# Performance work log

Measured on AMD Instinct MI355X. Metric: run time of the kernel, lower is better.

The kernel has to match this reference:

```python
import jax, jax.numpy as jnp
import numpy as np

NUM_EMBEDDINGS = 8192
EMBEDDING_DIM = 256
COMMITMENT_COST = 0.25


def setup_inputs() -> dict:
    key = jax.random.key(0)
    k1, k2 = jax.random.split(key)
    inputs = jax.random.normal(k1, (32, 32, 32, EMBEDDING_DIM), dtype=jnp.float32)
    # flax nn.initializers.uniform(scale=1/num_embeddings) -> U[0, scale)
    embeddings = jax.random.uniform(
        k2, (NUM_EMBEDDINGS, EMBEDDING_DIM), dtype=jnp.float32,
        minval=0.0, maxval=1.0 / NUM_EMBEDDINGS)
    return {"inputs": inputs, "embeddings": embeddings}


def reference(inputs, embeddings):
    flat_input = inputs.reshape(-1, EMBEDDING_DIM)  # [N, D]
    distances = (jnp.sum(flat_input ** 2, axis=1, keepdims=True)
                 - 2.0 * jnp.dot(flat_input, embeddings.T)
                 + jnp.sum(embeddings ** 2, axis=1)[None, :])
    encoding_indices = jnp.argmin(distances, axis=1)  # [N]
    quantized = embeddings[encoding_indices]  # [N, D]

    e_latent_loss = jnp.mean((jax.lax.stop_gradient(quantized) - flat_input) ** 2)
    q_latent_loss = jnp.mean((quantized - jax.lax.stop_gradient(flat_input)) ** 2)
    vq_loss = q_latent_loss + COMMITMENT_COST * e_latent_loss

    # straight-through estimator
    quantized_st = flat_input + jax.lax.stop_gradient(quantized - flat_input)
    quantized_st = quantized_st.reshape(inputs.shape)

    # perplexity via codebook usage histogram (avoids materializing one-hot)
    counts = jnp.zeros((NUM_EMBEDDINGS,), dtype=flat_input.dtype).at[encoding_indices].add(1.0)
    avg_probs = counts / flat_input.shape[0]
    perplexity = jnp.exp(-jnp.sum(avg_probs * jnp.log(avg_probs + 1e-10)))

    return quantized_st, vq_loss, perplexity, encoding_indices
```

## Files before the change

kernel.cpp:

```cpp
#include <hip/hip_runtime.h>
#include <math.h>

#pragma clang fp contract(off)

#define N_ROWS 32768
#define DIM    256
#define K_EMB  8192
#define BCAP   2048
#define NSUB   256

typedef float  f32x4  __attribute__((ext_vector_type(4)));
typedef short  bf16x8 __attribute__((ext_vector_type(8)));

__device__ __forceinline__ void gl_lds16(const uint4* g, uint4* l) {
  __builtin_amdgcn_global_load_lds(
      (const __attribute__((address_space(1))) unsigned int*)g,
      (__attribute__((address_space(3))) unsigned int*)l,
      16, 0, 0);
}

__device__ __forceinline__ unsigned bf_rne(float f) {
  unsigned u = __float_as_uint(f);
  return (u + 0x7fffu + ((u >> 16) & 1u)) >> 16;
}
__device__ __forceinline__ unsigned pack2(float lo, float hi) {
  return bf_rne(lo) | (bf_rne(hi) << 16);
}

__device__ __forceinline__ float np_pw128_sumsq(const float* __restrict__ a) {
  float4 v0 = *(const float4*)(a);
  float4 v1 = *(const float4*)(a + 4);
  float r0 = v0.x*v0.x, r1 = v0.y*v0.y, r2 = v0.z*v0.z, r3 = v0.w*v0.w;
  float r4 = v1.x*v1.x, r5 = v1.y*v1.y, r6 = v1.z*v1.z, r7 = v1.w*v1.w;
  for (int i = 8; i < 128; i += 8) {
    float4 w0 = *(const float4*)(a + i);
    float4 w1 = *(const float4*)(a + i + 4);
    r0 += w0.x*w0.x; r1 += w0.y*w0.y; r2 += w0.z*w0.z; r3 += w0.w*w0.w;
    r4 += w1.x*w1.x; r5 += w1.y*w1.y; r6 += w1.z*w1.z; r7 += w1.w*w1.w;
  }
  return ((r0+r1)+(r2+r3))+((r4+r5)+(r6+r7));
}

__global__ __launch_bounds__(256) void vq_sumsq(const float* __restrict__ src,
                                                float* __restrict__ dst, int nrows) {
  int gid  = blockIdx.x * 256 + threadIdx.x;
  int row  = gid >> 1, half = gid & 1;
  if (row >= nrows) return;
  float s = np_pw128_sumsq(src + (size_t)row * DIM + half * 128);
  float o = __shfl_xor(s, 1);
  if (half == 0) dst[row] = s + o;
}

__global__ __launch_bounds__(256) void vq_init(unsigned* __restrict__ hist,
                                               unsigned* __restrict__ bcnt,
                                               unsigned* __restrict__ ovf,
                                               unsigned long long* __restrict__ best) {
  int i = blockIdx.x * 256 + threadIdx.x;
  ovf[i]  = 0u;
  best[i] = ~0ull;
  if (i < K_EMB) hist[i] = 0u;
  if (i < NSUB)  bcnt[i] = 0u;
}

__global__ __launch_bounds__(256) void vq_cvt_frag(const float* __restrict__ E,
                                                   uint4* __restrict__ Eb) {
  int t = blockIdx.x * 256 + threadIdx.x;
  int tile = t >> 6, l = t & 63;
  int cfg = tile >> 3, ks = tile & 7;
  int code = cfg * 16 + (l & 15);
  int k0 = (ks * 4 + (l >> 4)) * 8;
  const float4* src = (const float4*)(E + (size_t)code * DIM + k0);
  float4 a = src[0], b = src[1];
  uint4 o;
  o.x = pack2(a.x, a.y); o.y = pack2(a.z, a.w);
  o.z = pack2(b.x, b.y); o.w = pack2(b.z, b.w);
  Eb[t] = o;
}

__global__ __launch_bounds__(512)
__attribute__((amdgpu_waves_per_eu(4, 4)))
void vq_mfma_slice(
    const float* __restrict__ X, const uint4* __restrict__ Eb,
    unsigned short* __restrict__ submax_g) {
  __shared__ __align__(16) unsigned short es[64 * 256];
  __shared__ unsigned short sh[2][64][128];

  const int tid   = threadIdx.x;
  const int lane  = tid & 63, w = tid >> 6;
  const int lr    = lane & 15, lg = lane >> 4;
  const int wcg   = w & 1;
  const int wxg   = w >> 1;
  const int rb    = blockIdx.x >> 1;
  const int slice = blockIdx.x & 1;
  const int row0  = rb * 128;

  bf16x8 bx[2][8];
#pragma unroll
  for (int cf = 0; cf < 2; ++cf) {
    const float* xr = X + (size_t)(row0 + wxg * 32 + cf * 16 + lr) * DIM;
#pragma unroll
    for (int ks = 0; ks < 8; ++ks) {
      int k0 = (ks * 4 + lg) * 8;
      float4 a = *(const float4*)(xr + k0);
      float4 b = *(const float4*)(xr + k0 + 4);
      uint4 o;
      o.x = pack2(a.x, a.y); o.y = pack2(a.z, a.w);
      o.z = pack2(b.x, b.y); o.w = pack2(b.z, b.w);
      bx[cf][ks] = *(bf16x8*)&o;
    }
  }

  const uint4* ebase = Eb + (size_t)slice * 131072;

  for (int c = 0; c < 64; ++c) {
    __syncthreads();
#pragma unroll
    for (int i = 0; i < 4; ++i) {
      int u = tid + i * 512;
      gl_lds16(ebase + (size_t)c * 2048 + u, ((uint4*)es) + u);
    }
    __syncthreads();

    f32x4 acc[2][2];
#pragma unroll
    for (int rf = 0; rf < 2; ++rf)
#pragma unroll
      for (int cf = 0; cf < 2; ++cf)
        acc[rf][cf] = (f32x4){0.f, 0.f, 0.f, 0.f};

#pragma unroll
    for (int ks = 0; ks < 8; ++ks) {
      bf16x8 ev0 = *(const bf16x8*)(es + (((wcg * 2 + 0) * 8 + ks) * 64 + lane) * 8);
      bf16x8 ev1 = *(const bf16x8*)(es + (((wcg * 2 + 1) * 8 + ks) * 64 + lane) * 8);
      acc[0][0] = __builtin_amdgcn_mfma_f32_16x16x32_bf16(ev0, bx[0][ks], acc[0][0], 0, 0, 0);
      acc[0][1] = __builtin_amdgcn_mfma_f32_16x16x32_bf16(ev0, bx[1][ks], acc[0][1], 0, 0, 0);
      acc[1][0] = __builtin_amdgcn_mfma_f32_16x16x32_bf16(ev1, bx[0][ks], acc[1][0], 0, 0, 0);
      acc[1][1] = __builtin_amdgcn_mfma_f32_16x16x32_bf16(ev1, bx[1][ks], acc[1][1], 0, 0, 0);
    }

#pragma unroll
    for (int cf = 0; cf < 2; ++cf) {
      float m = acc[0][cf][0];
#pragma unroll
      for (int rf = 0; rf < 2; ++rf)
#pragma unroll
        for (int rg = 0; rg < 4; ++rg)
          if (rf | rg) m = fmaxf(m, acc[rf][cf][rg]);
      m = fmaxf(m, __shfl_xor(m, 16));
      m = fmaxf(m, __shfl_xor(m, 32));
      if (lg == 0) {
        int qi = (int)((m + 0.0625f) * 524288.0f);
        qi = qi < 0 ? 0 : (qi > 65535 ? 65535 : qi);
        sh[wcg][c][wxg * 32 + cf * 16 + lr] = (unsigned short)qi;
      }
    }
  }
  __syncthreads();

  {
    int r = tid & 127, g = tid >> 7;
    unsigned short* dst = submax_g + (size_t)(row0 + r) * NSUB + slice * 128 + g * 32;
#pragma unroll
    for (int i = 0; i < 32; ++i) {
      int sl = g * 32 + i;
      dst[i] = sh[sl & 1][sl >> 1][r];
    }
  }
}

__global__ __launch_bounds__(256) void vq_flag(
    const unsigned short* __restrict__ submax_g, const float* __restrict__ A,
    unsigned* __restrict__ bcnt, unsigned short* __restrict__ buckets,
    unsigned* __restrict__ ovf) {
  __shared__ unsigned cntA[NSUB], baseS[NSUB], cntC[NSUB];
  const int t   = threadIdx.x;
  const int row = blockIdx.x * 256 + t;
  cntA[t] = 0u; cntC[t] = 0u;
  __syncthreads();

  const unsigned short* sr = submax_g + (size_t)row * NSUB;
  int mq = 0;
  for (int s = 0; s < NSUB; ++s) {
    int q = sr[s];
    mq = q > mq ? q : mq;
  }
  const int wq   = (int)((sqrtf(A[row]) * 4e-6f + 9.6e-5f) * 524288.0f) + 2;
  const int thrq = mq - wq;

  for (int s = 0; s < NSUB; ++s)
    if ((int)sr[s] >= thrq) atomicAdd(&cntA[s], 1u);
  __syncthreads();

  baseS[t] = atomicAdd(&bcnt[t], cntA[t]);
  __syncthreads();

  for (int s = 0; s < NSUB; ++s) {
    if ((int)sr[s] >= thrq) {
      unsigned p = baseS[s] + atomicAdd(&cntC[s], 1u);
      if (p < BCAP) buckets[s * BCAP + p] = (unsigned short)row;
      else          ovf[row] = 1u;
    }
  }
}

__global__ __launch_bounds__(256) void vq_exact(
    const float* __restrict__ X, const float* __restrict__ E,
    const float* __restrict__ A, const float* __restrict__ C,
    const unsigned* __restrict__ bcnt, const unsigned short* __restrict__ buckets,
    unsigned long long* __restrict__ best) {
  __shared__ float e_lds[32][260];
  __shared__ float xr[4][4][256];
  const int tid  = threadIdx.x;
  const int lane = tid & 63, w = tid >> 6;
  const int bk   = blockIdx.x >> 2, q4 = blockIdx.x & 3;

#pragma unroll
  for (int i = 0; i < 8; ++i) {
    int u = tid + i * 256;
    int code = u >> 6, koff = (u & 63) * 4;
    float4 v = *(const float4*)(E + (size_t)(bk * 32 + code) * DIM + koff);
    *(float4*)(&e_lds[code][koff]) = v;
  }
  __syncthreads();

  int n = (int)bcnt[bk]; if (n > BCAP) n = BCAP;
  const int   half = lane >> 5, c32 = lane & 31;
  const int   j  = bk * 32 + c32;
  const float cj = C[j];

  for (int p0 = q4 * 16 + w * 4; p0 < n; p0 += 64) {
    int valid[4], rows[4];
#pragma unroll
    for (int k = 0; k < 4; ++k) {
      int pk = p0 + k;
      valid[k] = (pk < n);
      rows[k]  = buckets[(size_t)bk * BCAP + (pk < n ? pk : p0)];
    }
#pragma unroll
    for (int k = 0; k < 4; ++k)
      *(float4*)(&xr[w][k][lane * 4]) =
          *(const float4*)(X + (size_t)rows[k] * DIM + lane * 4);
    asm volatile("s_waitcnt lgkmcnt(0)" ::: "memory");

    float acc0 = 0.f, acc1 = 0.f;
    const float* xa = &xr[w][half][0];
    const float* xb = &xr[w][half + 2][0];
#pragma unroll 4
    for (int kq = 0; kq < 64; ++kq) {
      float4 ev = *(const float4*)(&e_lds[c32][kq * 4]);
      float4 x0 = *(const float4*)(xa + kq * 4);
      float4 x1 = *(const float4*)(xb + kq * 4);
      acc0 = fmaf(x0.x, ev.x, acc0); acc0 = fmaf(x0.y, ev.y, acc0);
      acc0 = fmaf(x0.z, ev.z, acc0); acc0 = fmaf(x0.w, ev.w, acc0);
      acc1 = fmaf(x1.x, ev.x, acc1); acc1 = fmaf(x1.y, ev.y, acc1);
      acc1 = fmaf(x1.z, ev.z, acc1); acc1 = fmaf(x1.w, ev.w, acc1);
    }
    float d0 = (A[rows[half]]     - 2.0f * acc0) + cj;
    float d1 = (A[rows[half + 2]] - 2.0f * acc1) + cj;
    int   j0 = j, j1 = j;
#pragma unroll
    for (int mm = 1; mm < 32; mm <<= 1) {
      float od = __shfl_xor(d0, mm); int oj = __shfl_xor(j0, mm);
      if (od < d0 || (od == d0 && oj < j0)) { d0 = od; j0 = oj; }
      od = __shfl_xor(d1, mm); oj = __shfl_xor(j1, mm);
      if (od < d1 || (od == d1 && oj < j1)) { d1 = od; j1 = oj; }
    }
    if (c32 == 0) {
      if (valid[half])
        atomicMin(&best[rows[half]],
                  ((unsigned long long)__float_as_uint(d0) << 32) | (unsigned)j0);
      if (valid[half + 2])
        atomicMin(&best[rows[half + 2]],
                  ((unsigned long long)__float_as_uint(d1) << 32) | (unsigned)j1);
    }
  }
}

__global__ __launch_bounds__(256) void vq_finish(
    const float* __restrict__ X, const float* __restrict__ E,
    const float* __restrict__ A, const float* __restrict__ C,
    const unsigned* __restrict__ ovf, const unsigned long long* __restrict__ best,
    int* __restrict__ idx_out, float* __restrict__ idxf_out) {
  int row  = blockIdx.x * 4 + (threadIdx.x >> 6);
  int lane = threadIdx.x & 63;
  if (!ovf[row]) {
    if (lane == 0) {
      int j = (int)(best[row] & 0xffffffffu);
      idx_out[row]  = j;
      idxf_out[row] = (float)j;
    }
    return;
  }
  const float a_r = A[row];
  const float4* X4 = (const float4*)(X + (size_t)row * DIM);
  float bd = INFINITY; int bj = 0x7fffffff;
  for (int j = lane; j < K_EMB; j += 64) {
    const float4* E4 = (const float4*)(E + (size_t)j * DIM);
    float acc = 0.f;
    for (int kb = 0; kb < 64; ++kb) {
      float4 xv = X4[kb], ev = E4[kb];
      acc = fmaf(xv.x, ev.x, acc); acc = fmaf(xv.y, ev.y, acc);
      acc = fmaf(xv.z, ev.z, acc); acc = fmaf(xv.w, ev.w, acc);
    }
    float d = (a_r - 2.0f * acc) + C[j];
    if (d < bd || (d == bd && j < bj)) { bd = d; bj = j; }
  }
  for (int m = 1; m < 64; m <<= 1) {
    float od = __shfl_xor(bd, m);
    int   oj = __shfl_xor(bj, m);
    if (od < bd || (od == bd && oj < bj)) { bd = od; bj = oj; }
  }
  if (lane == 0) { idx_out[row] = bj; idxf_out[row] = (float)bj; }
}

__global__ __launch_bounds__(256) void vq_argmin(const float* __restrict__ X,
                                                 const float* __restrict__ E,
                                                 const float* __restrict__ A,
                                                 const float* __restrict__ C,
                                                 int* __restrict__ idx_out,
                                                 float* __restrict__ idxf_out) {
  __shared__ float4 xs4[64 * 64];
  const int tid  = threadIdx.x;
  const int rl   = tid >> 2;
  const int cg   = tid & 3;
  const int row0 = blockIdx.x * 64;

  const float4* Xg = (const float4*)(X + (size_t)row0 * DIM);
  for (int it = 0; it < 16; ++it) {
    int f4 = tid + it * 256;
    float4 v = Xg[f4];
    int r = f4 >> 6, kb = f4 & 63;
    xs4[r * 64 + (kb ^ (r & 7))] = v;
  }
  __syncthreads();

  const float a_r = A[row0 + rl];
  const int   swq = rl & 7;
  const float4* xrow = xs4 + rl * 64;

  float bd = INFINITY;
  int   bj = 0x7fffffff;

  for (int tile = 0; tile < K_EMB; tile += 16) {
    const int j0 = tile + cg * 4;
    const float4* e0 = (const float4*)(E + (size_t)(j0 + 0) * DIM);
    const float4* e1 = (const float4*)(E + (size_t)(j0 + 1) * DIM);
    const float4* e2 = (const float4*)(E + (size_t)(j0 + 2) * DIM);
    const float4* e3 = (const float4*)(E + (size_t)(j0 + 3) * DIM);
    float acc0 = 0.f, acc1 = 0.f, acc2 = 0.f, acc3 = 0.f;
#pragma unroll 4
    for (int kb = 0; kb < 64; ++kb) {
      const float4 xv = xrow[kb ^ swq];
      const float4 q0 = e0[kb], q1 = e1[kb], q2 = e2[kb], q3 = e3[kb];
      acc0 = fmaf(xv.x, q0.x, acc0); acc0 = fmaf(xv.y, q0.y, acc0);
      acc0 = fmaf(xv.z, q0.z, acc0); acc0 = fmaf(xv.w, q0.w, acc0);
      acc1 = fmaf(xv.x, q1.x, acc1); acc1 = fmaf(xv.y, q1.y, acc1);
      acc1 = fmaf(xv.z, q1.z, acc1); acc1 = fmaf(xv.w, q1.w, acc1);
      acc2 = fmaf(xv.x, q2.x, acc2); acc2 = fmaf(xv.y, q2.y, acc2);
      acc2 = fmaf(xv.z, q2.z, acc2); acc2 = fmaf(xv.w, q2.w, acc2);
      acc3 = fmaf(xv.x, q3.x, acc3); acc3 = fmaf(xv.y, q3.y, acc3);
      acc3 = fmaf(xv.z, q3.z, acc3); acc3 = fmaf(xv.w, q3.w, acc3);
    }
    const float d0 = (a_r - 2.0f * acc0) + C[j0 + 0];
    const float d1 = (a_r - 2.0f * acc1) + C[j0 + 1];
    const float d2 = (a_r - 2.0f * acc2) + C[j0 + 2];
    const float d3 = (a_r - 2.0f * acc3) + C[j0 + 3];
    if (d0 < bd) { bd = d0; bj = j0 + 0; }
    if (d1 < bd) { bd = d1; bj = j0 + 1; }
    if (d2 < bd) { bd = d2; bj = j0 + 2; }
    if (d3 < bd) { bd = d3; bj = j0 + 3; }
  }
  for (int m = 1; m < 4; m <<= 1) {
    float od = __shfl_xor(bd, m);
    int   oj = __shfl_xor(bj, m);
    if (od < bd || (od == bd && oj < bj)) { bd = od; bj = oj; }
  }
  if (cg == 0) {
    int row = row0 + rl;
    idx_out[row]  = bj;
    idxf_out[row] = (float)bj;
  }
}

__global__ __launch_bounds__(256) void vq_quant(const float* __restrict__ X,
                                                const float* __restrict__ E,
                                                const int* __restrict__ idx,
                                                float* __restrict__ out_qst,
                                                double* __restrict__ partials) {
  int gid  = blockIdx.x * 256 + threadIdx.x;
  int base = gid * 4;
  int row  = base >> 8;
  int k    = base & 255;
  int j    = idx[row];
  const float4 xv = *(const float4*)(X + (size_t)base);
  const float4 ev = *(const float4*)(E + (size_t)j * DIM + k);
  float4 o;
  float d0 = ev.x - xv.x, d1 = ev.y - xv.y, d2 = ev.z - xv.z, d3 = ev.w - xv.w;
  o.x = xv.x + d0; o.y = xv.y + d1; o.z = xv.z + d2; o.w = xv.w + d3;
  double s = (double)d0 * d0 + (double)d1 * d1 + (double)d2 * d2 + (double)d3 * d3;
  *(float4*)(out_qst + (size_t)base) = o;

  for (int m = 32; m; m >>= 1) s += __shfl_xor(s, m);
  __shared__ double wsum[4];
  int lane = threadIdx.x & 63, w = threadIdx.x >> 6;
  if (lane == 0) wsum[w] = s;
  __syncthreads();
  if (threadIdx.x == 0)
    partials[blockIdx.x] = (wsum[0] + wsum[1]) + (wsum[2] + wsum[3]);
}

__global__ void vq_zero(unsigned* counts) {
  int i = blockIdx.x * 256 + threadIdx.x;
  if (i < K_EMB) counts[i] = 0u;
}

__global__ void vq_hist(const int* __restrict__ idx, unsigned* __restrict__ counts) {
  int i = blockIdx.x * 256 + threadIdx.x;
  if (i < N_ROWS) atomicAdd(&counts[idx[i]], 1u);
}

__global__ __launch_bounds__(256) void vq_scalars(const double* __restrict__ partials,
                                                  const unsigned* __restrict__ counts,
                                                  float* __restrict__ out_loss,
                                                  float* __restrict__ out_perp) {
  __shared__ double red[256];
  int t = threadIdx.x;
  double s = 0.0;
  for (int i = t; i < 8192; i += 256) s += partials[i];
  red[t] = s;
  __syncthreads();
  for (int o = 128; o; o >>= 1) { if (t < o) red[t] += red[t + o]; __syncthreads(); }
  double mse = red[0] / (double)((size_t)N_ROWS * DIM);
  __syncthreads();

  double p = 0.0;
  for (int i = t; i < K_EMB; i += 256) {
    double pr = (double)counts[i] / (double)N_ROWS;
    p += pr * log(pr + 1e-10);
  }
  red[t] = p;
  __syncthreads();
  for (int o = 128; o; o >>= 1) { if (t < o) red[t] += red[t + o]; __syncthreads(); }
  if (t == 0) {
    float m = (float)mse;
    out_loss[0] = m + 0.25f * m;
    out_perp[0] = (float)exp(-red[0]);
  }
}

extern "C" void kernel_launch(void* const* d_in, const int* in_sizes, int n_in,
                              void* d_out, int out_size, void* d_ws, size_t ws_size,
                              hipStream_t stream) {
  const float* X = (const float*)d_in[0];
  const float* E = (const float*)d_in[1];
  float* out  = (float*)d_out;
  float* qst  = out;
  float* loss = out + 8388608;
  float* perp = out + 8388609;
  float* idxf = out + 8388610;

  float*    A        = (float*)d_ws;
  float*    C        = (float*)((char*)d_ws + 131072);
  int*      idx      = (int*)((char*)d_ws + 163840);
  unsigned* hist     = (unsigned*)((char*)d_ws + 294912);
  double*   partials = (double*)((char*)d_ws + 327680);

  vq_sumsq <<<256, 256, 0, stream>>>(X, A, N_ROWS);
  vq_sumsq <<<64,  256, 0, stream>>>(E, C, K_EMB);

  if (ws_size >= 22807552) {
    unsigned long long* best = (unsigned long long*)((char*)d_ws + 393216);
    unsigned* ovf          = (unsigned*)((char*)d_ws + 655360);
    unsigned* bcnt         = (unsigned*)((char*)d_ws + 786432);
    unsigned short* bucket = (unsigned short*)((char*)d_ws + 787456);
    uint4*    Eb           = (uint4*)((char*)d_ws + 1836032);
    unsigned short* sm     = (unsigned short*)((char*)d_ws + 6030336);

    vq_init       <<<128,  256, 0, stream>>>(hist, bcnt, ovf, best);
    vq_cvt_frag   <<<1024, 256, 0, stream>>>(E, Eb);
    vq_mfma_slice <<<512,  512, 0, stream>>>(X, Eb, sm);
    vq_flag       <<<128,  256, 0, stream>>>(sm, A, bcnt, bucket, ovf);
    vq_exact      <<<1024, 256, 0, stream>>>(X, E, A, C, bcnt, bucket, best);
    vq_finish     <<<8192, 256, 0, stream>>>(X, E, A, C, ovf, best, idx, idxf);
  } else {
    vq_zero   <<<32,  256, 0, stream>>>(hist);
    vq_argmin <<<512, 256, 0, stream>>>(X, E, A, C, idx, idxf);
  }

  vq_quant  <<<8192, 256, 0, stream>>>(X, E, idx, qst, partials);
  vq_hist   <<<128,  256, 0, stream>>>(idx, hist);
  vq_scalars<<<1,    256, 0, stream>>>(partials, hist, loss, perp);
}
```

Measured before the change: 369.4 us.

## Double-buffer codebook tiles and enlarge per-wave row tile in MFMA screening kernel

The MFMA screening kernel now runs with 256 threads per block, and each wave handles 64 rows instead of 32, so each LDS codebook fragment feeds twice as many MFMAs. The codebook tile in LDS is double-buffered: the next chunk is prefetched with global_load_lds while the current one is computed, leaving one barrier per iteration instead of two. Sub-maxima are written directly to global memory in a transposed [sub][row] layout, replacing the LDS staging buffer, and vq_flag reads that layout with coalesced per-row loads. The costs are more registers per thread (occupancy drops to 2 waves per EU) and doubled LDS for the codebook tile.

```diff
diff --git a/kernel.cpp b/kernel.cpp
--- a/kernel.cpp
+++ b/kernel.cpp
@@ -77,13 +77,12 @@
   Eb[t] = o;
 }
 
-__global__ __launch_bounds__(512)
-__attribute__((amdgpu_waves_per_eu(4, 4)))
+__global__ __launch_bounds__(256)
+__attribute__((amdgpu_waves_per_eu(2, 2)))
 void vq_mfma_slice(
     const float* __restrict__ X, const uint4* __restrict__ Eb,
-    unsigned short* __restrict__ submax_g) {
-  __shared__ __align__(16) unsigned short es[64 * 256];
-  __shared__ unsigned short sh[2][64][128];
+    unsigned short* __restrict__ submax_t) {
+  __shared__ __align__(16) unsigned short es[2][64 * 256];
 
   const int tid   = threadIdx.x;
   const int lane  = tid & 63, w = tid >> 6;
@@ -94,10 +93,18 @@
   const int slice = blockIdx.x & 1;
   const int row0  = rb * 128;
 
-  bf16x8 bx[2][8];
-#pragma unroll
-  for (int cf = 0; cf < 2; ++cf) {
-    const float* xr = X + (size_t)(row0 + wxg * 32 + cf * 16 + lr) * DIM;
+  const uint4* ebase = Eb + (size_t)slice * 131072;
+
+#pragma unroll
+  for (int i = 0; i < 8; ++i) {
+    int u = tid + i * 256;
+    gl_lds16(ebase + u, ((uint4*)&es[0][0]) + u);
+  }
+
+  bf16x8 bx[4][8];
+#pragma unroll
+  for (int rf = 0; rf < 4; ++rf) {
+    const float* xr = X + (size_t)(row0 + wxg * 64 + rf * 16 + lr) * DIM;
 #pragma unroll
     for (int ks = 0; ks < 8; ++ks) {
       int k0 = (ks * 4 + lg) * 8;
@@ -106,70 +113,65 @@
       uint4 o;
       o.x = pack2(a.x, a.y); o.y = pack2(a.z, a.w);
       o.z = pack2(b.x, b.y); o.w = pack2(b.z, b.w);
-      bx[cf][ks] = *(bf16x8*)&o;
-    }
-  }
-
-  const uint4* ebase = Eb + (size_t)slice * 131072;
+      bx[rf][ks] = *(bf16x8*)&o;
+    }
+  }
+  __syncthreads();
 
   for (int c = 0; c < 64; ++c) {
-    __syncthreads();
-#pragma unroll
-    for (int i = 0; i < 4; ++i) {
-      int u = tid + i * 512;
-      gl_lds16(ebase + (size_t)c * 2048 + u, ((uint4*)es) + u);
-    }
-    __syncthreads();
-
-    f32x4 acc[2][2];
-#pragma unroll
-    for (int rf = 0; rf < 2; ++rf)
-#pragma unroll
-      for (int cf = 0; cf < 2; ++cf)
-        acc[rf][cf] = (f32x4){0.f, 0.f, 0.f, 0.f};
-
+    const int cur = c & 1;
+    if (c + 1 < 64) {
+#pragma unroll
+      for (int i = 0; i < 8; ++i) {
+        int u = tid + i * 256;
+        gl_lds16(ebase + (size_t)(c + 1) * 2048 + u, ((uint4*)&es[cur ^ 1][0]) + u);
+      }
+    }
+
+    f32x4 acc[2][4];
+#pragma unroll
+    for (int ce = 0; ce < 2; ++ce)
+#pragma unroll
+      for (int rf = 0; rf < 4; ++rf)
+        acc[ce][rf] = (f32x4){0.f, 0.f, 0.f, 0.f};
+
+    const unsigned short* eb = &es[cur][0];
 #pragma unroll
     for (int ks = 0; ks < 8; ++ks) {
-      bf16x8 ev0 = *(const bf16x8*)(es + (((wcg * 2 + 0) * 8 + ks) * 64 + lane) * 8);
-      bf16x8 ev1 = *(const bf16x8*)(es + (((wcg * 2 + 1) * 8 + ks) * 64 + lane) * 8);
-      acc[0][0] = __builtin_amdgcn_mfma_f32_16x16x32_bf16(ev0, bx[0][ks], acc[0][0], 0, 0, 0);
-      acc[0][1] = __builtin_amdgcn_mfma_f32_16x16x32_bf16(ev0, bx[1][ks], acc[0][1], 0, 0, 0);
-      acc[1][0] = __builtin_amdgcn_mfma_f32_16x16x32_bf16(ev1, bx[0][ks], acc[1][0], 0, 0, 0);
-      acc[1][1] = __builtin_amdgcn_mfma_f32_16x16x32_bf16(ev1, bx[1][ks], acc[1][1], 0, 0, 0);
-    }
-
-#pragma unroll
-    for (int cf = 0; cf < 2; ++cf) {
-      float m = acc[0][cf][0];
-#pragma unroll
-      for (int rf = 0; rf < 2; ++rf)
+      bf16x8 ev0 = *(const bf16x8*)(eb + (((wcg * 2 + 0) * 8 + ks) * 64 + lane) * 8);
+      bf16x8 ev1 = *(const bf16x8*)(eb + (((wcg * 2 + 1) * 8 + ks) * 64 + lane) * 8);
+#pragma unroll
+      for (int rf = 0; rf < 4; ++rf) {
+        acc[0][rf] = __builtin_amdgcn_mfma_f32_16x16x32_bf16(ev0, bx[rf][ks], acc[0][rf], 0, 0, 0);
+        acc[1][rf] = __builtin_amdgcn_mfma_f32_16x16x32_bf16(ev1, bx[rf][ks], acc[1][rf], 0, 0, 0);
+      }
+    }
+
+    const int sub = slice * 128 + c * 2 + wcg;
+#pragma unroll
+    for (int rf = 0; rf < 4; ++rf) {
+      float m = acc[0][rf][0];
+#pragma unroll
+      for (int ce = 0; ce < 2; ++ce)
 #pragma unroll
         for (int rg = 0; rg < 4; ++rg)
-          if (rf | rg) m = fmaxf(m, acc[rf][cf][rg]);
+          if (ce | rg) m = fmaxf(m, acc[ce][rf][rg]);
       m = fmaxf(m, __shfl_xor(m, 16));
       m = fmaxf(m, __shfl_xor(m, 32));
       if (lg == 0) {
         int qi = (int)((m + 0.0625f) * 524288.0f);
         qi = qi < 0 ? 0 : (qi > 65535 ? 65535 : qi);
-        sh[wcg][c][wxg * 32 + cf * 16 + lr] = (unsigned short)qi;
+        submax_t[(size_t)sub * N_ROWS + row0 + wxg * 64 + rf * 16 + lr] =
+            (unsigned short)qi;
       }
     }
-  }
-  __syncthreads();
-
-  {
-    int r = tid & 127, g = tid >> 7;
-    unsigned short* dst = submax_g + (size_t)(row0 + r) * NSUB + slice * 128 + g * 32;
-#pragma unroll
-    for (int i = 0; i < 32; ++i) {
-      int sl = g * 32 + i;
-      dst[i] = sh[sl & 1][sl >> 1][r];
-    }
+
+    __syncthreads();
   }
 }
 
 __global__ __launch_bounds__(256) void vq_flag(
-    const unsigned short* __restrict__ submax_g, const float* __restrict__ A,
+    const unsigned short* __restrict__ submax_t, const float* __restrict__ A,
     unsigned* __restrict__ bcnt, unsigned short* __restrict__ buckets,
     unsigned* __restrict__ ovf) {
   __shared__ unsigned cntA[NSUB], baseS[NSUB], cntC[NSUB];
@@ -178,24 +180,23 @@
   cntA[t] = 0u; cntC[t] = 0u;
   __syncthreads();
 
-  const unsigned short* sr = submax_g + (size_t)row * NSUB;
   int mq = 0;
   for (int s = 0; s < NSUB; ++s) {
-    int q = sr[s];
+    int q = submax_t[(size_t)s * N_ROWS + row];
     mq = q > mq ? q : mq;
   }
   const int wq   = (int)((sqrtf(A[row]) * 4e-6f + 9.6e-5f) * 524288.0f) + 2;
   const int thrq = mq - wq;
 
   for (int s = 0; s < NSUB; ++s)
-    if ((int)sr[s] >= thrq) atomicAdd(&cntA[s], 1u);
+    if ((int)submax_t[(size_t)s * N_ROWS + row] >= thrq) atomicAdd(&cntA[s], 1u);
   __syncthreads();
 
   baseS[t] = atomicAdd(&bcnt[t], cntA[t]);
   __syncthreads();
 
   for (int s = 0; s < NSUB; ++s) {
-    if ((int)sr[s] >= thrq) {
+    if ((int)submax_t[(size_t)s * N_ROWS + row] >= thrq) {
       unsigned p = baseS[s] + atomicAdd(&cntC[s], 1u);
       if (p < BCAP) buckets[s * BCAP + p] = (unsigned short)row;
       else          ovf[row] = 1u;
@@ -478,7 +479,7 @@
 
     vq_init       <<<128,  256, 0, stream>>>(hist, bcnt, ovf, best);
     vq_cvt_frag   <<<1024, 256, 0, stream>>>(E, Eb);
-    vq_mfma_slice <<<512,  512, 0, stream>>>(X, Eb, sm);
+    vq_mfma_slice <<<512,  256, 0, stream>>>(X, Eb, sm);
     vq_flag       <<<128,  256, 0, stream>>>(sm, A, bcnt, bucket, ovf);
     vq_exact      <<<1024, 256, 0, stream>>>(X, E, A, C, bcnt, bucket, best);
     vq_finish     <<<8192, 256, 0, stream>>>(X, E, A, C, ovf, best, idx, idxf);
```

New measurement: 358.7 us. 2.9% less time.
